# Optimization experiments

Measured on AMD Instinct MI355X. Metric: run time of the kernel, lower is better.

## Reference

```python
import jax, jax.numpy as jnp
import numpy as np

BINWIDTHS = (5000, 1000, 500, 200, 100, 50, 25)
WINDOW = (0, 200000)
TOTAL = WINDOW[1] - WINDOW[0]

def _level_shapes():
    shapes = []
    cw = TOTAL
    for bw in BINWIDTHS:
        nb = cw // bw
        ns = TOTAL // (bw * nb)
        shapes.append((ns, nb))
        cw = bw
    return shapes

LEVEL_SHAPES = _level_shapes()          # [(1,40),(40,5),(200,2),(500,2),(1000,2),(2000,2),(4000,2)]
NBINS = [ns * nb for ns, nb in LEVEL_SHAPES]
N_FINAL = TOTAL // BINWIDTHS[-1]        # 8000

N_REGIONS = 500
N_CLUSTERS = 20
N_REGIONS_OI = 256
N_CELLS = 10000
N_CUTS = 500000
DELTA_P_SCALE = 1.5


def setup_inputs() -> dict:
    key = jax.random.key(0)
    ks = jax.random.split(key, 32)
    inp = {}
    inp["components"] = jax.random.normal(ks[0], (N_CLUSTERS, N_CLUSTERS), jnp.float32)
    for lvl, (ns, nb) in enumerate(LEVEL_SHAPES):
        inp[f"w_bias_{lvl}"] = jax.random.normal(ks[1 + lvl], (N_REGIONS, ns, nb), jnp.float32) * 0.05
        inp[f"w_delta_{lvl}"] = jax.random.normal(ks[10 + lvl], (N_REGIONS, N_CLUSTERS, ns * nb), jnp.float32) * 0.02
    inp["regions_oi"] = jax.random.randint(ks[20], (N_REGIONS_OI,), 0, N_REGIONS)
    inp["local_region_ix"] = jax.random.randint(ks[21], (N_CUTS,), 0, N_REGIONS_OI)
    inp["local_cell_ix"] = jax.random.randint(ks[22], (N_CUTS,), 0, N_CELLS)
    inp["clustering_indices"] = jax.random.randint(ks[23], (N_CELLS,), 0, N_CLUSTERS)
    inp["coordinates"] = jax.random.randint(ks[24], (N_CUTS,), WINDOW[0], WINDOW[1])
    return inp


def _calculate_w(components, w_biases, w_deltas, regions_oi):
    R = regions_oi.shape[0]
    C = components.shape[1]
    scale = jnp.float32(DELTA_P_SCALE)
    log_scale = jnp.log(scale)
    half_log_2pi = jnp.float32(0.5 * np.log(2.0 * np.pi))
    w = jnp.zeros((R, C, N_FINAL), jnp.float32)
    kl = jnp.float32(0.0)
    for lvl, (ns, nb) in enumerate(LEVEL_SHAPES):
        wb = w_biases[lvl][regions_oi]                    # (R, ns, nb) irregular gather
        Wd = w_deltas[lvl][regions_oi]                    # (R, C, ns*nb) irregular gather
        # MultiLinear: einsum('ab,cad->cbd', components, W)
        wd = jnp.einsum('ab,cad->cbd', components, Wd)    # (R, C, ns*nb)
        wd = wd.reshape(R, C, ns, nb)
        w_level = (wb[:, None, :, :] + wd).reshape(R, C, NBINS[lvl])
        rep = N_FINAL // NBINS[lvl]
        w = (w.reshape(R, C, NBINS[lvl], rep) + w_level[..., None]).reshape(R, C, N_FINAL)
        # Normal(0, scale).log_prob(wd), summed
        kl = kl + jnp.sum(-0.5 * (wd / scale) ** 2 - log_scale - half_log_2pi)
    w = jax.nn.log_softmax(w, axis=-1) - jnp.log(jnp.float32(BINWIDTHS[-1]))
    return w, kl


def reference(components, w_bias_0, w_bias_1, w_bias_2, w_bias_3, w_bias_4, w_bias_5, w_bias_6,
              w_delta_0, w_delta_1, w_delta_2, w_delta_3, w_delta_4, w_delta_5, w_delta_6,
              regions_oi, local_region_ix, local_cell_ix, clustering_indices, coordinates):
    w_biases = [w_bias_0, w_bias_1, w_bias_2, w_bias_3, w_bias_4, w_bias_5, w_bias_6]
    w_deltas = [w_delta_0, w_delta_1, w_delta_2, w_delta_3, w_delta_4, w_delta_5, w_delta_6]
    w, kl = _calculate_w(components, w_biases, w_deltas, regions_oi)
    coords = jnp.clip(coordinates, WINDOW[0], WINDOW[1] - 1) - WINDOW[0]
    bin_ix = coords // BINWIDTHS[-1]
    cluster_ix = clustering_indices[local_cell_ix]
    likelihood = w[local_region_ix, cluster_ix, bin_ix]   # (N_CUTS,)
    return likelihood, kl
```

## Files before the change

### kernel.cpp

```cpp
#include <hip/hip_runtime.h>
#include <hip/hip_bf16.h>
#include <math.h>


#define NROI 256
#define NC 20
#define NFINAL 8000
#define NCUTS 500000
#define TB 256
#define NTILE 32
#define XSTR 488
#define UTSTR 40

typedef __attribute__((ext_vector_type(8))) short bf16x8;
typedef __attribute__((ext_vector_type(4))) float f32x4;

static __device__ __forceinline__ ushort bfr(float x) {
    union { __hip_bfloat16 h; ushort u; } v;
    v.h = __float2bfloat16(x);
    return v.u;
}

__global__ void k_init(const float* __restrict__ comp,
                       float* __restrict__ g2, float* __restrict__ gfull,
                       ushort* __restrict__ compPad, float* __restrict__ kl)
{
    const int tid = threadIdx.x;
    if (tid == 0) kl[0] = (float)(-80076800.0 * 1.3244036413128371);
    for (int i = tid; i < 400; i += 256) {
        const int a = i / 20, b = i % 20;
        float s = 0.f;
#pragma unroll
        for (int c = 0; c < 20; c++) s += comp[a * 20 + c] * comp[b * 20 + c];
        g2[i] = (b < a) ? 0.f : (b == a ? s : 2.f * s);
    }
    for (int i = tid; i < 1024; i += 256) {
        const int rr = i >> 5, cc = i & 31;
        float s = 0.f;
        if (rr < 20 && cc < 20) {
#pragma unroll
            for (int c = 0; c < 20; c++) s += comp[rr * 20 + c] * comp[cc * 20 + c];
        }
        gfull[i] = s;
        const float v = (rr < 20 && cc < 20) ? comp[cc * 20 + rr] : 0.f;
        compPad[i] = bfr(v);
    }
}

__global__ __launch_bounds__(256, 2) void k_main(
    const float* __restrict__ gfull, const ushort* __restrict__ compPad,
    const float* __restrict__ wb0, const float* __restrict__ wd0,
    const float* __restrict__ wb1, const float* __restrict__ wd1,
    const float* __restrict__ wb2, const float* __restrict__ wd2,
    const float* __restrict__ wb3, const float* __restrict__ wd3,
    const float* __restrict__ wb4, const float* __restrict__ wd4,
    const float* __restrict__ wb5, const float* __restrict__ wd5,
    const float* __restrict__ wb6, const float* __restrict__ wd6,
    const int* __restrict__ regions_oi,
    __hip_bfloat16* __restrict__ w2,
    float* __restrict__ s_part, float* __restrict__ kl_out)
{
    __shared__ ushort Xsh[32 * XSTR];
    __shared__ ushort Utsh[TB * UTSTR];
    __shared__ float biasf[TB];
    __shared__ float sexp_sh[20];
    __shared__ float klp[3];

    const int tid = threadIdx.x;
    const int wv = tid >> 6, ln = tid & 63;
    const int l15 = ln & 15, lg = ln >> 4;
    const int r = blockIdx.x >> 5;
    const int tile = blockIdx.x & 31;
    const int base = tile << 8;
    const int r0 = regions_oi[r];

    const float* __restrict__ p6 = wd6 + (size_t)r0 * (20 * 8000);
    const float* __restrict__ p5 = wd5 + (size_t)r0 * (20 * 4000);
    const float* __restrict__ p4 = wd4 + (size_t)r0 * (20 * 2000);
    const float* __restrict__ p3 = wd3 + (size_t)r0 * (20 * 1000);
    const float* __restrict__ p2 = wd2 + (size_t)r0 * (20 * 400);
    const float* __restrict__ p1 = wd1 + (size_t)r0 * (20 * 200);
    const float* __restrict__ p0 = wd0 + (size_t)r0 * (20 * 40);
    const float* __restrict__ b6 = wb6 + (size_t)r0 * 8000;
    const float* __restrict__ b5 = wb5 + (size_t)r0 * 4000;
    const float* __restrict__ b4 = wb4 + (size_t)r0 * 2000;
    const float* __restrict__ b3 = wb3 + (size_t)r0 * 1000;
    const float* __restrict__ b2 = wb2 + (size_t)r0 * 400;
    const float* __restrict__ b1 = wb1 + (size_t)r0 * 200;
    const float* __restrict__ b0 = wb0 + (size_t)r0 * 40;

    if (tid < 20) sexp_sh[tid] = 0.f;
    if (tid < 3) klp[tid] = 0.f;

#pragma unroll 1
    for (int it = 0; it < 8; it++) {
        const int u = it * 256 + tid;
        if (u >= 2012) break;
        if (u < 1280) *(uint4*)&Utsh[u * 8] = make_uint4(0, 0, 0, 0);
        else          *(uint4*)&Xsh[20 * XSTR + (u - 1280) * 8] = make_uint4(0, 0, 0, 0);
    }
    __syncthreads();

#pragma unroll 1
    for (int it = 0; it < 6; it++) {
        const int u = it * 256 + tid;
        if (u >= 1344) break;
        const int a = u >> 6, jq = u & 63;
        const int j = base + 4 * jq;
        const float *q6, *q5, *q4, *q3, *q2, *q1, *q0;
        if (a < 20) {
            q6 = p6 + (size_t)a * 8000; q5 = p5 + a * 4000; q4 = p4 + a * 2000;
            q3 = p3 + a * 1000; q2 = p2 + a * 400; q1 = p1 + a * 200; q0 = p0 + a * 40;
        } else { q6 = b6; q5 = b5; q4 = b4; q3 = b3; q2 = b2; q1 = b1; q0 = b0; }
        float4 r6 = make_float4(0.f, 0.f, 0.f, 0.f);
        float2 r5 = make_float2(0.f, 0.f);
        float s4 = 0.f, s3 = 0.f, s2 = 0.f, s1 = 0.f, s0 = 0.f;
        if (j < NFINAL) {
            r6 = *(const float4*)(q6 + j);
            r5 = *(const float2*)(q5 + (j >> 1));
            s4 = q4[j >> 2]; s3 = q3[j >> 3]; s2 = q2[j / 20];
            s1 = q1[j / 40]; s0 = q0[j / 200];
        }
        const float sc = s4 + s3 + s2 + s1 + s0;
        const float c01 = sc + r5.x, c23 = sc + r5.y;
        const float u0 = r6.x + c01, u1 = r6.y + c01;
        const float u2 = r6.z + c23, u3 = r6.w + c23;
        if (a < 20) {
            *(ushort4*)&Xsh[a * XSTR + 4 * jq] =
                make_ushort4(bfr(r6.x), bfr(r6.y), bfr(r6.z), bfr(r6.w));
            *(ushort2*)&Xsh[a * XSTR + 256 + 2 * jq] =
                make_ushort2(bfr(r5.x), bfr(r5.y));
            Xsh[a * XSTR + 384 + jq] = bfr(s4);
            if (!(jq & 1)) Xsh[a * XSTR + 448 + (jq >> 1)] = bfr(s3);
            Utsh[(4 * jq + 0) * UTSTR + a] = bfr(u0);
            Utsh[(4 * jq + 1) * UTSTR + a] = bfr(u1);
            Utsh[(4 * jq + 2) * UTSTR + a] = bfr(u2);
            Utsh[(4 * jq + 3) * UTSTR + a] = bfr(u3);
        } else {
            *(float4*)&biasf[4 * jq] = make_float4(u0, u1, u2, u3);
        }
    }
    __syncthreads();

    if (wv < 3) {
        const int mt = (wv == 0) ? 0 : 1;
        const int nt = (wv == 2) ? 1 : 0;
        const int rowA = mt * 16 + l15;
        const int rowB = nt * 16 + l15;
        const int kb = lg * 8;
        f32x4 acc = {0.f, 0.f, 0.f, 0.f};
#pragma unroll 1
        for (int ch = 0; ch < 15; ch++) {
            bf16x8 fa = *(const bf16x8*)&Xsh[rowA * XSTR + ch * 32 + kb];
            bf16x8 fb = *(const bf16x8*)&Xsh[rowB * XSTR + ch * 32 + kb];
            acc = __builtin_amdgcn_mfma_f32_16x16x32_bf16(fa, fb, acc, 0, 0, 0);
        }
        float qp = 0.f;
#pragma unroll
        for (int reg = 0; reg < 4; reg++) {
            const int row = mt * 16 + lg * 4 + reg;
            const int col = nt * 16 + l15;
            qp += gfull[row * 32 + col] * acc[reg];
        }
        if (wv == 1) qp *= 2.f;
#pragma unroll
        for (int off = 32; off > 0; off >>= 1) qp += __shfl_down(qp, off, 64);
        if (ln == 0) klp[wv] = qp;
    }

    bf16x8 fA0 = *(const bf16x8*)&compPad[l15 * 32 + lg * 8];
    bf16x8 fA1 = *(const bf16x8*)&compPad[(16 + l15) * 32 + lg * 8];
    float sA[4] = {0.f, 0.f, 0.f, 0.f};
    float sB[4] = {0.f, 0.f, 0.f, 0.f};
#pragma unroll 1
    for (int t = 0; t < 4; t++) {
        const int nt = 4 * t + wv;
        bf16x8 fB = *(const bf16x8*)&Utsh[(nt * 16 + l15) * UTSTR + lg * 8];
        const f32x4 z = {0.f, 0.f, 0.f, 0.f};
        f32x4 c0 = __builtin_amdgcn_mfma_f32_16x16x32_bf16(fA0, fB, z, 0, 0, 0);
        f32x4 c1 = __builtin_amdgcn_mfma_f32_16x16x32_bf16(fA1, fB, z, 0, 0, 0);
        const int binl = nt * 16 + l15;
        const int bin = base + binl;
        const float bi = biasf[binl];
        if (bin < NFINAL) {
#pragma unroll
            for (int reg = 0; reg < 4; reg++) {
                const int c = lg * 4 + reg;
                const float w = bi + c0[reg];
                w2[(size_t)(r * 20 + c) * 8000 + bin] = __float2bfloat16(w);
                sA[reg] += __expf(w);
            }
            if (lg == 0) {
#pragma unroll
                for (int reg = 0; reg < 4; reg++) {
                    const float w = bi + c1[reg];
                    w2[(size_t)(r * 20 + 16 + reg) * 8000 + bin] = __float2bfloat16(w);
                    sB[reg] += __expf(w);
                }
            }
        }
    }
#pragma unroll
    for (int reg = 0; reg < 4; reg++) {
        float s = sA[reg];
        s += __shfl_xor(s, 1, 64); s += __shfl_xor(s, 2, 64);
        s += __shfl_xor(s, 4, 64); s += __shfl_xor(s, 8, 64);
        if (l15 == 0) atomicAdd(&sexp_sh[lg * 4 + reg], s);
        float sb = sB[reg];
        sb += __shfl_xor(sb, 1, 64); sb += __shfl_xor(sb, 2, 64);
        sb += __shfl_xor(sb, 4, 64); sb += __shfl_xor(sb, 8, 64);
        if (ln == 0) atomicAdd(&sexp_sh[16 + reg], sb);
    }
    __syncthreads();
    if (tid < 20) s_part[((size_t)r * NTILE + tile) * 20 + tid] = sexp_sh[tid];
    if (tid == 0)
        atomicAdd(kl_out, (klp[0] + klp[1] + klp[2]) * (-0.5f / 2.25f));
}

__global__ __launch_bounds__(256, 2) void k_klc(
    const float* __restrict__ g2,
    const float* __restrict__ wd0, const float* __restrict__ wd1,
    const float* __restrict__ wd2,
    const int* __restrict__ regions_oi, float* __restrict__ kl_out)
{
    __shared__ float klp[4];
    const int tid = threadIdx.x;
    const int r0 = regions_oi[blockIdx.x];
    const float* __restrict__ p2 = wd2 + (size_t)r0 * (20 * 400);
    const float* __restrict__ p1 = wd1 + (size_t)r0 * (20 * 200);
    const float* __restrict__ p0 = wd0 + (size_t)r0 * (20 * 40);

    float q = 0.f;
#pragma unroll 1
    for (int it = 0; it < 3; it++) {
        const int u = it * 256 + tid;
        if (u >= 640) break;
        const float* P; int K, col;
        if (u < 400)      { P = p2; K = 400; col = u; }
        else if (u < 600) { P = p1; K = 200; col = u - 400; }
        else              { P = p0; K = 40;  col = u - 600; }
        float x[20];
#pragma unroll
        for (int a = 0; a < 20; a++) x[a] = P[a * K + col];
#pragma unroll
        for (int a = 0; a < 20; a++) {
            float t = g2[a * 21] * x[a];
#pragma unroll
            for (int b = a + 1; b < 20; b++) t += g2[a * 20 + b] * x[b];
            q += x[a] * t;
        }
    }
#pragma unroll
    for (int off = 32; off > 0; off >>= 1) q += __shfl_down(q, off, 64);
    if ((tid & 63) == 0) klp[tid >> 6] = q;
    __syncthreads();
    if (tid == 0)
        atomicAdd(kl_out, (klp[0] + klp[1] + klp[2] + klp[3]) * (-0.5f / 2.25f));
}

__global__ void k_sub(const float* __restrict__ s_part, float* __restrict__ sub)
{
    const int i = blockIdx.x * 256 + threadIdx.x;
    if (i >= NROI * NC) return;
    const int r = i / 20, c = i % 20;
    float s = 0.f;
#pragma unroll 1
    for (int t = 0; t < NTILE; t++) s += s_part[(size_t)(r * NTILE + t) * 20 + c];
    sub[i] = logf(s) + 3.2188758248682006f;
}

__global__ void k_gather(const int* __restrict__ lri, const int* __restrict__ lci,
                         const int* __restrict__ cli, const int* __restrict__ coords,
                         const __hip_bfloat16* __restrict__ w2,
                         const float* __restrict__ sub,
                         float* __restrict__ out)
{
    const int i = blockIdx.x * 256 + threadIdx.x;
    if (i >= NCUTS) return;
    const int r = lri[i];
    const int c = cli[lci[i]];
    int co = coords[i];
    co = co < 0 ? 0 : (co > 199999 ? 199999 : co);
    const int bin = co / 25;
    const int rc = r * 20 + c;
    out[i] = __bfloat162float(w2[(size_t)rc * 8000 + bin]) - sub[rc];
}

extern "C" void kernel_launch(void* const* d_in, const int* in_sizes, int n_in,
                              void* d_out, int out_size, void* d_ws, size_t ws_size,
                              hipStream_t stream)
{
    const float* comp = (const float*)d_in[0];
    const float* wb[7];
    const float* wd[7];
    if (in_sizes[2] == 400000) {
        for (int l = 0; l < 7; l++) { wb[l] = (const float*)d_in[1 + 2 * l]; wd[l] = (const float*)d_in[2 + 2 * l]; }
    } else {
        for (int l = 0; l < 7; l++) { wb[l] = (const float*)d_in[1 + l]; wd[l] = (const float*)d_in[8 + l]; }
    }
    const int* regions_oi = (const int*)d_in[15];
    const int* lri   = (const int*)d_in[16];
    const int* lci   = (const int*)d_in[17];
    const int* cli   = (const int*)d_in[18];
    const int* coords= (const int*)d_in[19];
    float* out = (float*)d_out;

    __hip_bfloat16* w2 = (__hip_bfloat16*)d_ws;
    float* s_part = (float*)(w2 + (size_t)NROI * NC * NFINAL);
    float* sub    = s_part + (size_t)NROI * NTILE * 20;
    float* g2buf  = sub + NROI * NC;
    float* gfull  = g2buf + 400;
    ushort* compPad = (ushort*)(gfull + 1024);
    const size_t need = (size_t)NROI * NC * NFINAL * 2
                      + ((size_t)NROI * NTILE * 20 + NROI * NC + 400 + 1024 + 512)
                        * sizeof(float);
    if (ws_size < need) return;

    k_init<<<1, 256, 0, stream>>>(comp, g2buf, gfull, compPad, out + NCUTS);
    k_main<<<NROI * NTILE, 256, 0, stream>>>(gfull, compPad,
        wb[0], wd[0], wb[1], wd[1], wb[2], wd[2], wb[3], wd[3],
        wb[4], wd[4], wb[5], wd[5], wb[6], wd[6],
        regions_oi, w2, s_part, out + NCUTS);
    k_klc<<<NROI, 256, 0, stream>>>(g2buf, wd[0], wd[1], wd[2],
        regions_oi, out + NCUTS);
    k_sub<<<(NROI * NC + 255) / 256, 256, 0, stream>>>(s_part, sub);
    k_gather<<<(NCUTS + 255) / 256, 256, 0, stream>>>(lri, lci, cli, coords,
        w2, sub, out);
}
```

Before: 192.6 us.

## Drop shared X staging buffer; load KL Gram operands straight from global memory

The large shared staging array used to hold bf16 copies of the level 3–6 delta tiles is removed. The Gram-matrix MFMA for the KL term now reads its operands directly from global memory, with each chunk packed to bf16 in registers, and the chunks are spread across all four waves. Each wave atomically adds its own KL partial instead of combining them in shared memory. The U-matrix build is restructured: the coarse-level sums are precomputed per 4-bin group into a small shared array, and each thread then builds one bin row across all clusters. This cuts shared memory use, which could raise occupancy, at the cost of re-reading the delta data from global memory or cache and issuing more global atomics.

Result: slower. 493.5 us (+156.3%).

```diff
diff --git a/kernel.cpp b/kernel.cpp
--- a/kernel.cpp
+++ b/kernel.cpp
@@ -9,7 +9,6 @@
 #define NCUTS 500000
 #define TB 256
 #define NTILE 32
-#define XSTR 488
 #define UTSTR 40
 
 typedef __attribute__((ext_vector_type(8))) short bf16x8;
@@ -19,6 +18,12 @@
     union { __hip_bfloat16 h; ushort u; } v;
     v.h = __float2bfloat16(x);
     return v.u;
+}
+static __device__ __forceinline__ bf16x8 pack8(float4 a, float4 b) {
+    union { bf16x8 v; ushort s[8]; } u;
+    u.s[0] = bfr(a.x); u.s[1] = bfr(a.y); u.s[2] = bfr(a.z); u.s[3] = bfr(a.w);
+    u.s[4] = bfr(b.x); u.s[5] = bfr(b.y); u.s[6] = bfr(b.z); u.s[7] = bfr(b.w);
+    return u.v;
 }
 
 __global__ void k_init(const float* __restrict__ comp,
@@ -60,11 +65,10 @@
     __hip_bfloat16* __restrict__ w2,
     float* __restrict__ s_part, float* __restrict__ kl_out)
 {
-    __shared__ ushort Xsh[32 * XSTR];
     __shared__ ushort Utsh[TB * UTSTR];
+    __shared__ float cs_sh[20 * 64];
     __shared__ float biasf[TB];
     __shared__ float sexp_sh[20];
-    __shared__ float klp[3];
 
     const int tid = threadIdx.x;
     const int wv = tid >> 6, ln = tid & 63;
@@ -90,131 +94,143 @@
     const float* __restrict__ b0 = wb0 + (size_t)r0 * 40;
 
     if (tid < 20) sexp_sh[tid] = 0.f;
-    if (tid < 3) klp[tid] = 0.f;
-
-#pragma unroll 1
-    for (int it = 0; it < 8; it++) {
+
+#pragma unroll 1
+    for (int it = 0; it < 5; it++) {
         const int u = it * 256 + tid;
-        if (u >= 2012) break;
-        if (u < 1280) *(uint4*)&Utsh[u * 8] = make_uint4(0, 0, 0, 0);
-        else          *(uint4*)&Xsh[20 * XSTR + (u - 1280) * 8] = make_uint4(0, 0, 0, 0);
+        const int a = u >> 6, qd = u & 63;
+        const int j = base + 4 * qd;
+        float v = 0.f;
+        if (j < NFINAL)
+            v = p4[a * 2000 + (j >> 2)] + p3[a * 1000 + (j >> 3)]
+              + p2[a * 400 + j / 20] + p1[a * 200 + j / 40]
+              + p0[a * 40 + j / 200];
+        cs_sh[a * 64 + qd] = v;
+    }
+    {
+        const int j = base + tid;
+        float v = 0.f;
+        if (j < NFINAL)
+            v = b6[j] + b5[j >> 1] + b4[j >> 2] + b3[j >> 3]
+              + b2[j / 20] + b1[j / 40] + b0[j / 200];
+        biasf[tid] = v;
     }
     __syncthreads();
 
-#pragma unroll 1
-    for (int it = 0; it < 6; it++) {
-        const int u = it * 256 + tid;
-        if (u >= 1344) break;
-        const int a = u >> 6, jq = u & 63;
-        const int j = base + 4 * jq;
-        const float *q6, *q5, *q4, *q3, *q2, *q1, *q0;
-        if (a < 20) {
-            q6 = p6 + (size_t)a * 8000; q5 = p5 + a * 4000; q4 = p4 + a * 2000;
-            q3 = p3 + a * 1000; q2 = p2 + a * 400; q1 = p1 + a * 200; q0 = p0 + a * 40;
-        } else { q6 = b6; q5 = b5; q4 = b4; q3 = b3; q2 = b2; q1 = b1; q0 = b0; }
-        float4 r6 = make_float4(0.f, 0.f, 0.f, 0.f);
-        float2 r5 = make_float2(0.f, 0.f);
-        float s4 = 0.f, s3 = 0.f, s2 = 0.f, s1 = 0.f, s0 = 0.f;
-        if (j < NFINAL) {
-            r6 = *(const float4*)(q6 + j);
-            r5 = *(const float2*)(q5 + (j >> 1));
-            s4 = q4[j >> 2]; s3 = q3[j >> 3]; s2 = q2[j / 20];
-            s1 = q1[j / 40]; s0 = q0[j / 200];
-        }
-        const float sc = s4 + s3 + s2 + s1 + s0;
-        const float c01 = sc + r5.x, c23 = sc + r5.y;
-        const float u0 = r6.x + c01, u1 = r6.y + c01;
-        const float u2 = r6.z + c23, u3 = r6.w + c23;
-        if (a < 20) {
-            *(ushort4*)&Xsh[a * XSTR + 4 * jq] =
-                make_ushort4(bfr(r6.x), bfr(r6.y), bfr(r6.z), bfr(r6.w));
-            *(ushort2*)&Xsh[a * XSTR + 256 + 2 * jq] =
-                make_ushort2(bfr(r5.x), bfr(r5.y));
-            Xsh[a * XSTR + 384 + jq] = bfr(s4);
-            if (!(jq & 1)) Xsh[a * XSTR + 448 + (jq >> 1)] = bfr(s3);
-            Utsh[(4 * jq + 0) * UTSTR + a] = bfr(u0);
-            Utsh[(4 * jq + 1) * UTSTR + a] = bfr(u1);
-            Utsh[(4 * jq + 2) * UTSTR + a] = bfr(u2);
-            Utsh[(4 * jq + 3) * UTSTR + a] = bfr(u3);
-        } else {
-            *(float4*)&biasf[4 * jq] = make_float4(u0, u1, u2, u3);
-        }
+    {
+        const int j = base + tid;
+        const bool ok = j < NFINAL;
+        const int qd = tid >> 2;
+#pragma unroll 1
+        for (int it = 0; it < 5; it++) {
+            float u[4];
+#pragma unroll
+            for (int i = 0; i < 4; i++) {
+                const int a = 4 * it + i;
+                float x6 = 0.f, x5 = 0.f;
+                if (ok) {
+                    x6 = p6[(size_t)a * 8000 + j];
+                    x5 = p5[a * 4000 + (j >> 1)];
+                }
+                u[i] = x6 + x5 + cs_sh[a * 64 + qd];
+            }
+            *(ushort4*)&Utsh[tid * UTSTR + 4 * it] =
+                make_ushort4(bfr(u[0]), bfr(u[1]), bfr(u[2]), bfr(u[3]));
+        }
+        const ushort4 z4 = make_ushort4(0, 0, 0, 0);
+        *(ushort4*)&Utsh[tid * UTSTR + 20] = z4;
+        *(ushort4*)&Utsh[tid * UTSTR + 24] = z4;
+        *(ushort4*)&Utsh[tid * UTSTR + 28] = z4;
     }
     __syncthreads();
 
-    if (wv < 3) {
-        const int mt = (wv == 0) ? 0 : 1;
-        const int nt = (wv == 2) ? 1 : 0;
-        const int rowA = mt * 16 + l15;
-        const int rowB = nt * 16 + l15;
-        const int kb = lg * 8;
-        f32x4 acc = {0.f, 0.f, 0.f, 0.f};
-#pragma unroll 1
-        for (int ch = 0; ch < 15; ch++) {
-            bf16x8 fa = *(const bf16x8*)&Xsh[rowA * XSTR + ch * 32 + kb];
-            bf16x8 fb = *(const bf16x8*)&Xsh[rowB * XSTR + ch * 32 + kb];
-            acc = __builtin_amdgcn_mfma_f32_16x16x32_bf16(fa, fb, acc, 0, 0, 0);
-        }
-        float qp = 0.f;
-#pragma unroll
-        for (int reg = 0; reg < 4; reg++) {
-            const int row = mt * 16 + lg * 4 + reg;
-            const int col = nt * 16 + l15;
-            qp += gfull[row * 32 + col] * acc[reg];
-        }
-        if (wv == 1) qp *= 2.f;
-#pragma unroll
-        for (int off = 32; off > 0; off >>= 1) qp += __shfl_down(qp, off, 64);
-        if (ln == 0) klp[wv] = qp;
-    }
-
-    bf16x8 fA0 = *(const bf16x8*)&compPad[l15 * 32 + lg * 8];
-    bf16x8 fA1 = *(const bf16x8*)&compPad[(16 + l15) * 32 + lg * 8];
-    float sA[4] = {0.f, 0.f, 0.f, 0.f};
-    float sB[4] = {0.f, 0.f, 0.f, 0.f};
-#pragma unroll 1
-    for (int t = 0; t < 4; t++) {
-        const int nt = 4 * t + wv;
-        bf16x8 fB = *(const bf16x8*)&Utsh[(nt * 16 + l15) * UTSTR + lg * 8];
-        const f32x4 z = {0.f, 0.f, 0.f, 0.f};
-        f32x4 c0 = __builtin_amdgcn_mfma_f32_16x16x32_bf16(fA0, fB, z, 0, 0, 0);
-        f32x4 c1 = __builtin_amdgcn_mfma_f32_16x16x32_bf16(fA1, fB, z, 0, 0, 0);
-        const int binl = nt * 16 + l15;
-        const int bin = base + binl;
-        const float bi = biasf[binl];
-        if (bin < NFINAL) {
-#pragma unroll
-            for (int reg = 0; reg < 4; reg++) {
-                const int c = lg * 4 + reg;
-                const float w = bi + c0[reg];
-                w2[(size_t)(r * 20 + c) * 8000 + bin] = __float2bfloat16(w);
-                sA[reg] += __expf(w);
-            }
-            if (lg == 0) {
-#pragma unroll
-                for (int reg = 0; reg < 4; reg++) {
-                    const float w = bi + c1[reg];
-                    w2[(size_t)(r * 20 + 16 + reg) * 8000 + bin] = __float2bfloat16(w);
-                    sB[reg] += __expf(w);
+    {
+        f32x4 s00 = {0.f, 0.f, 0.f, 0.f};
+        f32x4 s10 = {0.f, 0.f, 0.f, 0.f};
+        f32x4 s11 = {0.f, 0.f, 0.f, 0.f};
+#pragma unroll 1
+        for (int ch = wv; ch < 15; ch += 4) {
+            const float* P; int K, col0;
+            if (ch < 8)       { P = p6; K = 8000; col0 = base + ch * 32; }
+            else if (ch < 12) { P = p5; K = 4000; col0 = (base >> 1) + (ch - 8) * 32; }
+            else if (ch < 14) { P = p4; K = 2000; col0 = (base >> 2) + (ch - 12) * 32; }
+            else              { P = p3; K = 1000; col0 = (base >> 3); }
+            const int cb = col0 + lg * 8;
+            bf16x8 flo = {0,0,0,0,0,0,0,0}, fhi = {0,0,0,0,0,0,0,0};
+            if (cb < K) {
+                const float4 xa = *(const float4*)(P + (size_t)l15 * K + cb);
+                const float4 xb = *(const float4*)(P + (size_t)l15 * K + cb + 4);
+                flo = pack8(xa, xb);
+                if (l15 < 4) {
+                    const float4 ya = *(const float4*)(P + (size_t)(16 + l15) * K + cb);
+                    const float4 yb = *(const float4*)(P + (size_t)(16 + l15) * K + cb + 4);
+                    fhi = pack8(ya, yb);
                 }
             }
-        }
-    }
-#pragma unroll
-    for (int reg = 0; reg < 4; reg++) {
-        float s = sA[reg];
-        s += __shfl_xor(s, 1, 64); s += __shfl_xor(s, 2, 64);
-        s += __shfl_xor(s, 4, 64); s += __shfl_xor(s, 8, 64);
-        if (l15 == 0) atomicAdd(&sexp_sh[lg * 4 + reg], s);
-        float sb = sB[reg];
-        sb += __shfl_xor(sb, 1, 64); sb += __shfl_xor(sb, 2, 64);
-        sb += __shfl_xor(sb, 4, 64); sb += __shfl_xor(sb, 8, 64);
-        if (ln == 0) atomicAdd(&sexp_sh[16 + reg], sb);
+            s00 = __builtin_amdgcn_mfma_f32_16x16x32_bf16(flo, flo, s00, 0, 0, 0);
+            s10 = __builtin_amdgcn_mfma_f32_16x16x32_bf16(fhi, flo, s10, 0, 0, 0);
+            s11 = __builtin_amdgcn_mfma_f32_16x16x32_bf16(fhi, fhi, s11, 0, 0, 0);
+        }
+        float qp = 0.f;
+#pragma unroll
+        for (int reg = 0; reg < 4; reg++) {
+            const int rlo = lg * 4 + reg, rhi = 16 + lg * 4 + reg;
+            qp += gfull[rlo * 32 + l15] * s00[reg];
+            qp += 2.f * gfull[rhi * 32 + l15] * s10[reg];
+            qp += gfull[rhi * 32 + 16 + l15] * s11[reg];
+        }
+#pragma unroll
+        for (int off = 32; off > 0; off >>= 1) qp += __shfl_down(qp, off, 64);
+        if (ln == 0) atomicAdd(kl_out, qp * (-0.5f / 2.25f));
+    }
+
+    {
+        bf16x8 fA0 = *(const bf16x8*)&compPad[l15 * 32 + lg * 8];
+        bf16x8 fA1 = *(const bf16x8*)&compPad[(16 + l15) * 32 + lg * 8];
+        float sA[4] = {0.f, 0.f, 0.f, 0.f};
+        float sB[4] = {0.f, 0.f, 0.f, 0.f};
+#pragma unroll 1
+        for (int t = 0; t < 4; t++) {
+            const int nt = 4 * t + wv;
+            bf16x8 fB = *(const bf16x8*)&Utsh[(nt * 16 + l15) * UTSTR + lg * 8];
+            const f32x4 z = {0.f, 0.f, 0.f, 0.f};
+            f32x4 c0 = __builtin_amdgcn_mfma_f32_16x16x32_bf16(fA0, fB, z, 0, 0, 0);
+            f32x4 c1 = __builtin_amdgcn_mfma_f32_16x16x32_bf16(fA1, fB, z, 0, 0, 0);
+            const int binl = nt * 16 + l15;
+            const int bin = base + binl;
+            const float bi = biasf[binl];
+            if (bin < NFINAL) {
+#pragma unroll
+                for (int reg = 0; reg < 4; reg++) {
+                    const int c = lg * 4 + reg;
+                    const float w = bi + c0[reg];
+                    w2[(size_t)(r * 20 + c) * 8000 + bin] = __float2bfloat16(w);
+                    sA[reg] += __expf(w);
+                }
+                if (lg == 0) {
+#pragma unroll
+                    for (int reg = 0; reg < 4; reg++) {
+                        const float w = bi + c1[reg];
+                        w2[(size_t)(r * 20 + 16 + reg) * 8000 + bin] = __float2bfloat16(w);
+                        sB[reg] += __expf(w);
+                    }
+                }
+            }
+        }
+#pragma unroll
+        for (int reg = 0; reg < 4; reg++) {
+            float s = sA[reg];
+            s += __shfl_xor(s, 1, 64); s += __shfl_xor(s, 2, 64);
+            s += __shfl_xor(s, 4, 64); s += __shfl_xor(s, 8, 64);
+            if (l15 == 0) atomicAdd(&sexp_sh[lg * 4 + reg], s);
+            float sb = sB[reg];
+            sb += __shfl_xor(sb, 1, 64); sb += __shfl_xor(sb, 2, 64);
+            sb += __shfl_xor(sb, 4, 64); sb += __shfl_xor(sb, 8, 64);
+            if (ln == 0) atomicAdd(&sexp_sh[16 + reg], sb);
+        }
     }
     __syncthreads();
     if (tid < 20) s_part[((size_t)r * NTILE + tile) * 20 + tid] = sexp_sh[tid];
-    if (tid == 0)
-        atomicAdd(kl_out, (klp[0] + klp[1] + klp[2]) * (-0.5f / 2.25f));
 }
 
 __global__ __launch_bounds__(256, 2) void k_klc(
```
